# Performance work log

Measured on AMD Instinct MI355X. Metric: run time of the kernel, lower is better.

Reference implementation:

```python
import jax, jax.numpy as jnp
import numpy as np

B, G = 32, 8          # batch, num_genres
N, T = 64, 64         # notes_size, timestep_size (input)
D, O = 32, 32         # notes_out, timestep_out (output)


def setup_inputs() -> dict:
    key = jax.random.key(0)
    k1, k2, k3, k4, k5 = jax.random.split(key, 5)
    x = jax.random.normal(k1, (B, N, T), dtype=jnp.float32)
    y = jax.random.uniform(k2, (B, G), dtype=jnp.float32)
    weight = jax.random.normal(k3, (G, D, O, N, T), dtype=jnp.float32) * 0.02
    bias = jax.random.normal(k4, (D * O,), dtype=jnp.float32) * 0.02
    mask = jax.random.randint(k5, (O, T), 0, 2).astype(jnp.float32)
    return {"x": x, "y": y, "weight": weight, "bias": bias, "mask": mask}


def reference(x, y, weight, bias, mask):
    # Fused form of:
    #   mw  = einsum('gdont,ot->gdont', weight, mask)
    #   mw2 = einsum('gdont,bg->bdont', mw, y)      # huge intermediate avoided
    #   out = einsum('bnt,bdont->bdo', x, mw2) + bias
    mw = weight * mask[None, None, :, None, :]          # (g,d,o,n,t)
    xw = jnp.einsum('bnt,gdont->bgdo', x, mw)           # contract n,t first
    out = jnp.einsum('bg,bgdo->bdo', y, xw)             # (b,d,o)
    return out + bias.reshape(D, O)[None, :, :]
```

## Files before the change

### kernel.cpp

```cpp
#include <hip/hip_runtime.h>
#include <hip/hip_bf16.h>

typedef __bf16 bf16x8 __attribute__((ext_vector_type(8)));
typedef float f32x4 __attribute__((ext_vector_type(4)));

#define G 8
#define B 32
#define D 32
#define O 32
#define K 4096
#define T 64
#define KSPLIT 2
#define KCHUNK (K / KSPLIT)
#define BK 256
#define NSTEP (KCHUNK / BK)
#define MROWS 16

#define XB_ELEMS (B * K)

__global__ __launch_bounds__(256) void prep_and_init(const float* __restrict__ x,
                                                     const float* __restrict__ bias,
                                                     __bf16* __restrict__ xb,
                                                     float* __restrict__ out) {
    int tid = blockIdx.x * 256 + threadIdx.x;
    if (tid < 16384) {
        int b = (tid >> 2) & 31;
        int k = (tid >> 7) * 32 + (tid & 3) * 8;
        const float4 x0 = *(const float4*)(x + b * K + k);
        const float4 x1 = *(const float4*)(x + b * K + k + 4);
        bf16x8 r;
        r[0] = (__bf16)x0.x; r[1] = (__bf16)x0.y; r[2] = (__bf16)x0.z; r[3] = (__bf16)x0.w;
        r[4] = (__bf16)x1.x; r[5] = (__bf16)x1.y; r[6] = (__bf16)x1.z; r[7] = (__bf16)x1.w;
        *(bf16x8*)(xb + (size_t)tid * 8) = r;
    } else {
        int t2 = tid - 16384;
        out[t2] = bias[t2 & 1023];
    }
}

__global__ __launch_bounds__(128) void gemm_main(const float* __restrict__ W,
                                                 const __bf16* __restrict__ xb,
                                                 const float* __restrict__ mask,
                                                 const float* __restrict__ y,
                                                 float* __restrict__ out) {
    __shared__ float ldsW[2][MROWS * BK];
    const int d = blockIdx.x, g = blockIdx.y;
    const int oh = blockIdx.z & 1, ks = blockIdx.z >> 1;
    const int wid  = threadIdx.x >> 6;
    const int lane = threadIdx.x & 63;
    const int bh = wid;
    const int l15 = lane & 15, g16 = lane >> 4;

    const int lds_ro = l15 * 1024 + ((g16 * 32) ^ ((l15 & 7) * 16));

    const float* mrow = mask + (oh * 16 + l15) * T + g16 * 8;
    const float4 me0 = *(const float4*)(mrow);
    const float4 me1 = *(const float4*)(mrow + 4);
    const float4 mo0 = *(const float4*)(mrow + 32);
    const float4 mo1 = *(const float4*)(mrow + 36);

    const __bf16* xbl = xb + (size_t)(ks * (KCHUNK / 32)) * 1024
                           + (bh * 16 + l15) * 32 + g16 * 8;

    const size_t wrow0 = ((size_t)(g * D + d) * O + oh * 16 + 8 * wid) * K
                         + (size_t)ks * KCHUNK;

    f32x4 acc = {0.f, 0.f, 0.f, 0.f};

#define STAGE(buf, step)                                                          \
    {                                                                             \
        _Pragma("unroll")                                                         \
        for (int i = 0; i < 8; ++i) {                                             \
            const int row = 8 * wid + i;                                          \
            const char* src = (const char*)(W + wrow0 + (size_t)i * K             \
                                            + (size_t)(step) * BK)                \
                              + ((lane * 16) ^ (i * 16));                         \
            __builtin_amdgcn_global_load_lds(                                     \
                (const __attribute__((address_space(1))) void*)src,               \
                (__attribute__((address_space(3))) void*)((char*)&ldsW[buf][0]    \
                                                          + row * 1024),          \
                16, 0, 0);                                                        \
        }                                                                         \
    }

    bf16x8 xr[8];
#define XLOAD(step)                                                               \
    {                                                                             \
        _Pragma("unroll")                                                         \
        for (int s = 0; s < 8; ++s)                                               \
            xr[s] = *(const bf16x8*)(xbl + (size_t)(step) * 8192                  \
                                         + (size_t)s * 1024);                     \
    }

    STAGE(0, 0);

    #pragma unroll
    for (int step = 0; step < NSTEP; ++step) {
        const int cur = step & 1;

        XLOAD(step);
        __builtin_amdgcn_sched_barrier(0);
        if (step + 1 < NSTEP) {
            STAGE(cur ^ 1, step + 1);
            __builtin_amdgcn_sched_barrier(0);
            asm volatile("s_waitcnt vmcnt(8)" ::: "memory");
        } else {
            __builtin_amdgcn_sched_barrier(0);
            asm volatile("s_waitcnt vmcnt(0)" ::: "memory");
        }
        __builtin_amdgcn_s_barrier();
        __builtin_amdgcn_sched_barrier(0);

        const char* lb = (const char*)&ldsW[cur][0];
        #pragma unroll
        for (int s = 0; s < 8; ++s) {
            const int a0 = lds_ro + s * 128;
            const f32x4 alo = *(const f32x4*)(lb + a0);
            const f32x4 ahi = *(const f32x4*)(lb + (a0 ^ 16));
            const float4 ms0 = (s & 1) ? mo0 : me0;
            const float4 ms1 = (s & 1) ? mo1 : me1;
            bf16x8 af;
            af[0] = (__bf16)(alo[0] * ms0.x); af[1] = (__bf16)(alo[1] * ms0.y);
            af[2] = (__bf16)(alo[2] * ms0.z); af[3] = (__bf16)(alo[3] * ms0.w);
            af[4] = (__bf16)(ahi[0] * ms1.x); af[5] = (__bf16)(ahi[1] * ms1.y);
            af[6] = (__bf16)(ahi[2] * ms1.z); af[7] = (__bf16)(ahi[3] * ms1.w);
            acc = __builtin_amdgcn_mfma_f32_16x16x32_bf16(af, xr[s], acc, 0, 0, 0);
        }

        __builtin_amdgcn_sched_barrier(0);
        asm volatile("s_waitcnt lgkmcnt(0)" ::: "memory");
        __builtin_amdgcn_s_barrier();
    }
#undef STAGE
#undef XLOAD

    const int bg = bh * 16 + l15;
    const float yv = y[bg * G + g];
    float* op = out + bg * (D * O) + d * O + oh * 16;
    #pragma unroll
    for (int i = 0; i < 4; ++i)
        unsafeAtomicAdd(op + g16 * 4 + i, yv * acc[i]);
}

extern "C" void kernel_launch(void* const* d_in, const int* in_sizes, int n_in,
                              void* d_out, int out_size, void* d_ws, size_t ws_size,
                              hipStream_t stream) {
    const float* x    = (const float*)d_in[0];
    const float* y    = (const float*)d_in[1];
    const float* w    = (const float*)d_in[2];
    const float* bias = (const float*)d_in[3];
    const float* mask = (const float*)d_in[4];
    float* out = (float*)d_out;

    __bf16* xbp = (__bf16*)d_ws;

    prep_and_init<<<192, 256, 0, stream>>>(x, bias, xbp, out);
    gemm_main<<<dim3(D, G, 4), 128, 0, stream>>>(w, xbp, mask, y, out);
}
```

Measured before the change: 36.01 us.

## Use one wave per block covering both batch halves, dropping barriers

```diff
diff --git a/kernel.cpp b/kernel.cpp
--- a/kernel.cpp
+++ b/kernel.cpp
@@ -38,17 +38,15 @@
     }
 }
 
-__global__ __launch_bounds__(128) void gemm_main(const float* __restrict__ W,
-                                                 const __bf16* __restrict__ xb,
-                                                 const float* __restrict__ mask,
-                                                 const float* __restrict__ y,
-                                                 float* __restrict__ out) {
+__global__ __launch_bounds__(64) void gemm_main(const float* __restrict__ W,
+                                                const __bf16* __restrict__ xb,
+                                                const float* __restrict__ mask,
+                                                const float* __restrict__ y,
+                                                float* __restrict__ out) {
     __shared__ float ldsW[2][MROWS * BK];
     const int d = blockIdx.x, g = blockIdx.y;
     const int oh = blockIdx.z & 1, ks = blockIdx.z >> 1;
-    const int wid  = threadIdx.x >> 6;
-    const int lane = threadIdx.x & 63;
-    const int bh = wid;
+    const int lane = threadIdx.x;
     const int l15 = lane & 15, g16 = lane >> 4;
 
     const int lds_ro = l15 * 1024 + ((g16 * 32) ^ ((l15 & 7) * 16));
@@ -59,37 +57,37 @@
     const float4 mo0 = *(const float4*)(mrow + 32);
     const float4 mo1 = *(const float4*)(mrow + 36);
 
-    const __bf16* xbl = xb + (size_t)(ks * (KCHUNK / 32)) * 1024
-                           + (bh * 16 + l15) * 32 + g16 * 8;
+    const __bf16* xbl = xb + (size_t)(ks * (KCHUNK / 32)) * 1024 + l15 * 32 + g16 * 8;
 
-    const size_t wrow0 = ((size_t)(g * D + d) * O + oh * 16 + 8 * wid) * K
-                         + (size_t)ks * KCHUNK;
+    const size_t wrow0 = ((size_t)(g * D + d) * O + oh * 16) * K + (size_t)ks * KCHUNK;
 
-    f32x4 acc = {0.f, 0.f, 0.f, 0.f};
+    f32x4 acc0 = {0.f, 0.f, 0.f, 0.f};
+    f32x4 acc1 = {0.f, 0.f, 0.f, 0.f};
 
 #define STAGE(buf, step)                                                          \
     {                                                                             \
         _Pragma("unroll")                                                         \
-        for (int i = 0; i < 8; ++i) {                                             \
-            const int row = 8 * wid + i;                                          \
+        for (int i = 0; i < MROWS; ++i) {                                         \
             const char* src = (const char*)(W + wrow0 + (size_t)i * K             \
                                             + (size_t)(step) * BK)                \
-                              + ((lane * 16) ^ (i * 16));                         \
+                              + ((lane * 16) ^ ((i & 7) * 16));                   \
             __builtin_amdgcn_global_load_lds(                                     \
                 (const __attribute__((address_space(1))) void*)src,               \
                 (__attribute__((address_space(3))) void*)((char*)&ldsW[buf][0]    \
-                                                          + row * 1024),          \
+                                                          + i * 1024),            \
                 16, 0, 0);                                                        \
         }                                                                         \
     }
 
-    bf16x8 xr[8];
+    bf16x8 xr[2][8];
 #define XLOAD(step)                                                               \
     {                                                                             \
         _Pragma("unroll")                                                         \
-        for (int s = 0; s < 8; ++s)                                               \
-            xr[s] = *(const bf16x8*)(xbl + (size_t)(step) * 8192                  \
-                                         + (size_t)s * 1024);                     \
+        for (int h = 0; h < 2; ++h)                                               \
+            _Pragma("unroll")                                                     \
+            for (int s = 0; s < 8; ++s)                                           \
+                xr[h][s] = *(const bf16x8*)(xbl + (size_t)(step) * 8192           \
+                                                + (size_t)s * 1024 + h * 512);    \
     }
 
     STAGE(0, 0);
@@ -103,12 +101,11 @@
         if (step + 1 < NSTEP) {
             STAGE(cur ^ 1, step + 1);
             __builtin_amdgcn_sched_barrier(0);
-            asm volatile("s_waitcnt vmcnt(8)" ::: "memory");
+            asm volatile("s_waitcnt vmcnt(16)" ::: "memory");
         } else {
             __builtin_amdgcn_sched_barrier(0);
             asm volatile("s_waitcnt vmcnt(0)" ::: "memory");
         }
-        __builtin_amdgcn_s_barrier();
         __builtin_amdgcn_sched_barrier(0);
 
         const char* lb = (const char*)&ldsW[cur][0];
@@ -124,22 +121,23 @@
             af[2] = (__bf16)(alo[2] * ms0.z); af[3] = (__bf16)(alo[3] * ms0.w);
             af[4] = (__bf16)(ahi[0] * ms1.x); af[5] = (__bf16)(ahi[1] * ms1.y);
             af[6] = (__bf16)(ahi[2] * ms1.z); af[7] = (__bf16)(ahi[3] * ms1.w);
-            acc = __builtin_amdgcn_mfma_f32_16x16x32_bf16(af, xr[s], acc, 0, 0, 0);
+            acc0 = __builtin_amdgcn_mfma_f32_16x16x32_bf16(af, xr[0][s], acc0, 0, 0, 0);
+            acc1 = __builtin_amdgcn_mfma_f32_16x16x32_bf16(af, xr[1][s], acc1, 0, 0, 0);
         }
-
         __builtin_amdgcn_sched_barrier(0);
-        asm volatile("s_waitcnt lgkmcnt(0)" ::: "memory");
-        __builtin_amdgcn_s_barrier();
     }
 #undef STAGE
 #undef XLOAD
 
-    const int bg = bh * 16 + l15;
-    const float yv = y[bg * G + g];
-    float* op = out + bg * (D * O) + d * O + oh * 16;
+    const float yv0 = y[l15 * G + g];
+    const float yv1 = y[(16 + l15) * G + g];
+    float* op0 = out + l15 * (D * O) + d * O + oh * 16 + g16 * 4;
+    float* op1 = op0 + 16 * (D * O);
     #pragma unroll
-    for (int i = 0; i < 4; ++i)
-        unsafeAtomicAdd(op + g16 * 4 + i, yv * acc[i]);
+    for (int i = 0; i < 4; ++i) {
+        unsafeAtomicAdd(op0 + i, yv0 * acc0[i]);
+        unsafeAtomicAdd(op1 + i, yv1 * acc1[i]);
+    }
 }
 
 extern "C" void kernel_launch(void* const* d_in, const int* in_sizes, int n_in,
@@ -155,5 +153,5 @@
     __bf16* xbp = (__bf16*)d_ws;
 
     prep_and_init<<<192, 256, 0, stream>>>(x, bias, xbp, out);
-    gemm_main<<<dim3(D, G, 4), 128, 0, stream>>>(w, xbp, mask, y, out);
+    gemm_main<<<dim3(D, G, 4), 64, 0, stream>>>(w, xbp, mask, y, out);
 }
```

Result: slower. 37.42 us (+3.9%).
